# Performance work log

Hardware: AMD Instinct MI355X
Metric: run time of the kernel (lower is better)

## Reference

```python
import jax, jax.numpy as jnp
import numpy as np

H = 512      # hidden_size
L = 3        # num_layers
V = 4        # vocab / input_size
E = 64       # embedding_dim
B = 64       # batch
T = 512      # sequence length


def _rnn_layer(xs, h0, w_ih, w_hh, b_ih, b_hh):
    # xs: [T, B, D_in], h0: [B, H] -> (ys [T,B,H], hT [B,H])
    def step(h, x):
        h_new = jnp.tanh(x @ w_ih.T + b_ih + h @ w_hh.T + b_hh)
        return h_new, h_new
    hT, ys = jax.lax.scan(step, h0, xs)
    return ys, hT


def setup_inputs() -> dict:
    key = jax.random.key(0)
    ks = jax.random.split(key, 12)
    s = 1.0 / np.sqrt(H)  # torch RNN default init scale
    inp = {
        "x": jax.random.normal(ks[0], (B, T, V), dtype=jnp.float32),
        "emb": jax.random.normal(ks[1], (V, E), dtype=jnp.float32),
        # encoder RNN: layer 0 has input dim E, layers 1..2 have input dim H
        "enc_w_ih0": jax.random.uniform(ks[2], (H, E), jnp.float32, -s, s),
        "enc_w_ih_rest": jax.random.uniform(ks[3], (L - 1, H, H), jnp.float32, -s, s),
        "enc_w_hh": jax.random.uniform(ks[4], (L, H, H), jnp.float32, -s, s),
        "enc_b_ih": jax.random.uniform(ks[5], (L, H), jnp.float32, -s, s),
        "enc_b_hh": jax.random.uniform(ks[6], (L, H), jnp.float32, -s, s),
        # decoder RNN: all layers have input dim H
        "dec_w_ih": jax.random.uniform(ks[7], (L, H, H), jnp.float32, -s, s),
        "dec_w_hh": jax.random.uniform(ks[8], (L, H, H), jnp.float32, -s, s),
        "dec_b_ih": jax.random.uniform(ks[9], (L, H), jnp.float32, -s, s),
        "dec_b_hh": jax.random.uniform(ks[10], (L, H), jnp.float32, -s, s),
        "proj_w": jax.random.uniform(ks[11], (V, H), jnp.float32, -s, s),
    }
    return inp


def reference(x, emb, enc_w_ih0, enc_w_ih_rest, enc_w_hh, enc_b_ih, enc_b_hh,
              dec_w_ih, dec_w_hh, dec_b_ih, dec_b_hh, proj_w):
    # ---- Encoder ----
    # x_reduced_info slice is empty (FIRST_NONFUNCTIONAL_REDUCED_TOKEN_INDEX == len(VOCAB_REDUCED)),
    # so encoder RNN input is just the embedding of argmax(x).
    idx = jnp.argmax(x, axis=2)            # [B, T] int
    e = emb[idx]                           # [B, T, E]
    xs = jnp.transpose(e, (1, 0, 2))       # [T, B, E] (time-major for scan)

    h0 = jnp.zeros((B, H), dtype=x.dtype)
    enc_finals = []
    ys, hT = _rnn_layer(xs, h0, enc_w_ih0, enc_w_hh[0], enc_b_ih[0], enc_b_hh[0])
    enc_finals.append(hT)
    for l in range(1, L):
        ys, hT = _rnn_layer(ys, h0, enc_w_ih_rest[l - 1], enc_w_hh[l], enc_b_ih[l], enc_b_hh[l])
        enc_finals.append(hT)
    enc_h = jnp.stack(enc_finals, axis=0)  # [L, B, H]

    dec_h0 = jnp.flip(enc_h, axis=0)       # reverse_input_h=True
    x0 = jnp.zeros((B, H), dtype=x.dtype)

    def dec_step(carry, _):
        xin, hs = carry                    # xin [B,H], hs [L,B,H]
        new_hs = []
        cur = xin
        for l in range(L):
            h = jnp.tanh(cur @ dec_w_ih[l].T + dec_b_ih[l]
                         + hs[l] @ dec_w_hh[l].T + dec_b_hh[l])
            new_hs.append(h)
            cur = h
        out = jax.nn.log_softmax(cur @ proj_w.T, axis=-1)  # [B, V]
        return (cur, jnp.stack(new_hs, axis=0)), out

    _, outs = jax.lax.scan(dec_step, (x0, dec_h0), None, length=T)  # [T, B, V]
    return jnp.transpose(outs, (1, 0, 2))  # [B, T, V]
```

## Files before the change

kernel.cpp:

```cpp
#include <hip/hip_runtime.h>
#include <cmath>

#define HH 512
#define NV 4
#define ED 64
#define NB 64
#define NT 512

#define NWG  256
#define NTHR 512
#define WPG  32
#define RPG  8
#define CPW  16

#define HPAR (NB * HH)

#define IN0_OFF 0
#define IN1_OFF (8 * 1024)
#define LDS_FLOATS (IN1_OFF + 8 * 1024)
#define LDS_BYTES_ALLOC 98304

#define WS_INT_FLOATS 9216
#define FLAG(g, cb) (((g) * 32 + (cb)) * 32)

static __device__ __forceinline__ float gld(const float* p) {
  return __hip_atomic_load(p, __ATOMIC_RELAXED, __HIP_MEMORY_SCOPE_AGENT);
}
static __device__ __forceinline__ void gst(float* p, float v) {
  __hip_atomic_store(p, v, __ATOMIC_RELAXED, __HIP_MEMORY_SCOPE_AGENT);
}

static __device__ __forceinline__ void gbar(int* flags, int g, int cb, int ph) {
  asm volatile("s_waitcnt vmcnt(0)" ::: "memory");
  __syncthreads();
  if (threadIdx.x == 0)
    __hip_atomic_store(flags + FLAG(g, cb), ph, __ATOMIC_RELAXED,
                       __HIP_MEMORY_SCOPE_AGENT);
  if (threadIdx.x < 64) {
    const int* f = flags + FLAG(g, threadIdx.x & 31);
    while (__hip_atomic_load(f, __ATOMIC_RELAXED,
                             __HIP_MEMORY_SCOPE_AGENT) < ph)
      __builtin_amdgcn_s_sleep(1);
  }
  __syncthreads();
  asm volatile("" ::: "memory");
}

static __device__ __forceinline__ void gbar_all(int* ctr) {
  asm volatile("s_waitcnt vmcnt(0)" ::: "memory");
  __syncthreads();
  if (threadIdx.x == 0) {
    __hip_atomic_fetch_add(ctr, 1, __ATOMIC_RELAXED, __HIP_MEMORY_SCOPE_AGENT);
    while (__hip_atomic_load(ctr, __ATOMIC_RELAXED,
                             __HIP_MEMORY_SCOPE_AGENT) < NWG)
      __builtin_amdgcn_s_sleep(1);
  }
  __syncthreads();
  asm volatile("" ::: "memory");
}

template <bool COH>
static __device__ __forceinline__ void half_issue(const float* src, int row0,
                                                  float4 (&v)[2]) {
#pragma unroll
  for (int j = 0; j < 2; ++j) {
    const int qq = threadIdx.x + NTHR * j;
    const int row = qq >> 7, kq = qq & 127;
    const float* p = src + (size_t)(row0 + row) * HH + (kq << 2);
    if (COH) asm volatile("global_load_dwordx4 %0, %1, off sc0" : "=v"(v[j]) : "v"(p));
    else     asm volatile("global_load_dwordx4 %0, %1, off sc0 sc1" : "=v"(v[j]) : "v"(p));
  }
}
static __device__ __forceinline__ void half_commit(float* lds, int off,
                                                   int kofs, const float4 (&v)[2]) {
#pragma unroll
  for (int j = 0; j < 2; ++j) {
    const int qq = threadIdx.x + NTHR * j;
    const int row = qq >> 7, kq = qq & 127;
    *(float4*)(lds + off + row * 1024 + kofs + (kq << 2)) = v[j];
  }
}
static __device__ __forceinline__ void stage_half(float* lds, int off,
                                                  const float* src, int row0,
                                                  int kofs, int coh) {
  float4 v[2];
  if (coh) half_issue<true>(src, row0, v);
  else     half_issue<false>(src, row0, v);
  asm volatile("s_waitcnt vmcnt(0)" ::: "memory");
  __builtin_amdgcn_sched_barrier(0);
  half_commit(lds, off, kofs, v);
}

static __device__ __forceinline__ void unpk(float (&w)[16], int q, float4 v) {
  w[4*q+0] = v.x; w[4*q+1] = v.y; w[4*q+2] = v.z; w[4*q+3] = v.w;
}
static __device__ __forceinline__ void load_wq(float (&w)[16], const float* ih,
                                               const float* hh, int col, int ks) {
  unpk(w, 0, *(const float4*)(ih + (size_t)col * HH + ks * 4));
  unpk(w, 1, *(const float4*)(ih + (size_t)col * HH + 256 + ks * 4));
  unpk(w, 2, *(const float4*)(hh + (size_t)col * HH + ks * 4));
  unpk(w, 3, *(const float4*)(hh + (size_t)col * HH + 256 + ks * 4));
}
static __device__ __forceinline__ void load_wq0(float (&w)[16], const float* e,
                                                const float* hh, int col, int ks) {
  const float4 z = make_float4(0.f, 0.f, 0.f, 0.f);
  unpk(w, 0, (ks < 16) ? *(const float4*)(e + (size_t)col * ED + ks * 4)
                       : *(const float4*)(hh + (size_t)col * HH + (ks * 4 - 64)));
  unpk(w, 1, *(const float4*)(hh + (size_t)col * HH + 192 + ks * 4));
  unpk(w, 2, (ks < 16) ? *(const float4*)(hh + (size_t)col * HH + 448 + ks * 4) : z);
  unpk(w, 3, z);
}

static __device__ __forceinline__ void layer_tile(
    float* lds, int tile_off,
    const float (&wA)[16], const float (&wB)[16], float bA, float bB,
    float* dst, float* dst2, int row0, int colA, int coh) {
  const int lane = threadIdx.x & 63;
  const float* base = lds + tile_off + lane * 4;
  __syncthreads();
  float a[16];
#pragma unroll
  for (int v = 0; v < 16; ++v) a[v] = 0.f;
#pragma unroll
  for (int r = 0; r < 8; ++r) {
    const float* rb = base + r * 1024;
#pragma unroll
    for (int q = 0; q < 4; ++q) {
      const float4 iv = *(const float4*)(rb + q * 256);
      a[2*r+0] = fmaf(wA[4*q+0], iv.x, a[2*r+0]);
      a[2*r+0] = fmaf(wA[4*q+1], iv.y, a[2*r+0]);
      a[2*r+0] = fmaf(wA[4*q+2], iv.z, a[2*r+0]);
      a[2*r+0] = fmaf(wA[4*q+3], iv.w, a[2*r+0]);
      a[2*r+1] = fmaf(wB[4*q+0], iv.x, a[2*r+1]);
      a[2*r+1] = fmaf(wB[4*q+1], iv.y, a[2*r+1]);
      a[2*r+1] = fmaf(wB[4*q+2], iv.z, a[2*r+1]);
      a[2*r+1] = fmaf(wB[4*q+3], iv.w, a[2*r+1]);
    }
  }
  __syncthreads();
#pragma unroll
  for (int i = 0; i < 8; ++i) {
    const float send = (lane & 32) ? a[i] : a[i + 8];
    const float recv = __shfl_xor(send, 32);
    const float keep = (lane & 32) ? a[i + 8] : a[i];
    a[i] = keep + recv;
  }
#pragma unroll
  for (int i = 0; i < 4; ++i) {
    const float send = (lane & 16) ? a[i] : a[i + 4];
    const float recv = __shfl_xor(send, 16);
    const float keep = (lane & 16) ? a[i + 4] : a[i];
    a[i] = keep + recv;
  }
#pragma unroll
  for (int i = 0; i < 2; ++i) {
    const float send = (lane & 8) ? a[i] : a[i + 2];
    const float recv = __shfl_xor(send, 8);
    const float keep = (lane & 8) ? a[i + 2] : a[i];
    a[i] = keep + recv;
  }
  {
    const float send = (lane & 4) ? a[0] : a[1];
    const float recv = __shfl_xor(send, 4);
    const float keep = (lane & 4) ? a[1] : a[0];
    a[0] = keep + recv;
  }
  a[0] += __shfl_xor(a[0], 1);
  a[0] += __shfl_xor(a[0], 2);
  if ((lane & 3) == 0) {
    const int r  = ((lane >> 5) & 1) * 4 + ((lane >> 4) & 1) * 2 + ((lane >> 3) & 1);
    const int cc = (lane >> 2) & 1;
    const float h = tanhf(a[0] + (cc ? bB : bA));
    const size_t idx = (size_t)(row0 + r) * HH + colA + cc;
    if (coh) { dst[idx] = h; if (dst2) dst2[idx] = h; }
    else     { gst(dst + idx, h); if (dst2) gst(dst2 + idx, h); }
  }
}

static __device__ __forceinline__ void proj_row(const float* lds, int tile_off,
                                                int r_local, const float* projw,
                                                float* out, int row, int tt) {
  const int lane = threadIdx.x;
  const int v = lane & 3, kq = lane >> 2;
  float acc = 0.f;
#pragma unroll
  for (int i8 = 0; i8 < 8; ++i8) {
    const int k = (kq << 5) + (i8 << 2);
    const float4 iv = *(const float4*)(lds + tile_off + r_local * 1024 + k);
    const float4 wv = *(const float4*)(projw + (size_t)v * HH + k);
    acc = fmaf(iv.x, wv.x, acc);
    acc = fmaf(iv.y, wv.y, acc);
    acc = fmaf(iv.z, wv.z, acc);
    acc = fmaf(iv.w, wv.w, acc);
  }
  acc += __shfl_xor(acc, 4);
  acc += __shfl_xor(acc, 8);
  acc += __shfl_xor(acc, 16);
  acc += __shfl_xor(acc, 32);
  float m = fmaxf(acc, __shfl_xor(acc, 1));
  m = fmaxf(m, __shfl_xor(m, 2));
  const float e = expf(acc - m);
  float sum = e + __shfl_xor(e, 1);
  sum += __shfl_xor(sum, 2);
  const float res = acc - m - logf(sum);
  if (lane < 4) out[((size_t)row * NT + tt) * NV + lane] = res;
}

#define STG(off, src, kofs) stage_half(lds, off, src, row0, kofs, coh)
#define PF_ISSUE(src) \
  do { if (coh) half_issue<true>(src, row0, pf); \
       else     half_issue<false>(src, row0, pf); } while (0)

__global__ void __launch_bounds__(NTHR, 2) rnn_ae(
    const float* __restrict__ x, const float* __restrict__ emb,
    const float* __restrict__ ew_ih0, const float* __restrict__ ew_ihr,
    const float* __restrict__ ew_hh, const float* __restrict__ eb_ih,
    const float* __restrict__ eb_hh,
    const float* __restrict__ dw_ih, const float* __restrict__ dw_hh,
    const float* __restrict__ db_ih, const float* __restrict__ db_hh,
    const float* __restrict__ projw,
    float* __restrict__ out, float* __restrict__ ws) {
  extern __shared__ float lds[];

  const int tid = threadIdx.x;
  const int bid = blockIdx.x;
  const int g   = bid & 7;
  const int cb  = bid >> 3;
  const int row0 = g * RPG;
  const int col0 = cb * CPW;
  const int c   = tid >> 6;
  const int ks  = tid & 63;
  const int colA = col0 + 2 * c;
  const int colB = colA + 1;

  int* flags  = (int*)ws;
  int* gctr   = (int*)ws + 8192;
  int* xcdtab = (int*)ws + 8704;
  float* h0  = ws + WS_INT_FLOATS;
  float* h1  = h0 + 2 * HPAR;
  float* h2  = h1 + 2 * HPAR;
  float* e0  = h2 + 2 * HPAR;
  float* e1  = e0 + 2 * HPAR;
  float* e2  = e1 + 2 * HPAR;
  float* xfb = e2 + 2 * HPAR;
  int ph = 0;

  unsigned xcc;
  asm volatile("s_getreg_b32 %0, hwreg(HW_REG_XCC_ID)" : "=s"(xcc));
  if (tid == 0)
    __hip_atomic_store(xcdtab + bid, (int)xcc, __ATOMIC_RELAXED,
                       __HIP_MEMORY_SCOPE_AGENT);

  for (int i = tid; i < LDS_FLOATS; i += NTHR) lds[i] = 0.f;
  for (int i = cb * NTHR + tid; i < RPG * HH; i += WPG * NTHR) {
    const int r = i >> 9, cc = i & 511;
    const size_t o = HPAR + (size_t)(row0 + r) * HH + cc;
    gst(h0 + o, 0.f); gst(h1 + o, 0.f); gst(h2 + o, 0.f);
  }

  float wA0[16], wB0[16], wA1[16], wB1[16], wA2[16], wB2[16];
  float bA0, bB0, bA1, bB1, bA2, bB2;
  load_wq0(wA0, ew_ih0, ew_hh, colA, ks);
  load_wq0(wB0, ew_ih0, ew_hh, colB, ks);
  load_wq(wA1, ew_ihr,                ew_hh + (size_t)HH * HH,     colA, ks);
  load_wq(wB1, ew_ihr,                ew_hh + (size_t)HH * HH,     colB, ks);
  load_wq(wA2, ew_ihr + (size_t)HH * HH, ew_hh + (size_t)2 * HH * HH, colA, ks);
  load_wq(wB2, ew_ihr + (size_t)HH * HH, ew_hh + (size_t)2 * HH * HH, colB, ks);
  bA0 = eb_ih[0*HH + colA] + eb_hh[0*HH + colA];
  bB0 = eb_ih[0*HH + colB] + eb_hh[0*HH + colB];
  bA1 = eb_ih[1*HH + colA] + eb_hh[1*HH + colA];
  bB1 = eb_ih[1*HH + colB] + eb_hh[1*HH + colB];
  bA2 = eb_ih[2*HH + colA] + eb_hh[2*HH + colA];
  bB2 = eb_ih[2*HH + colB] + eb_hh[2*HH + colB];

  gbar_all(gctr);

  int coh = 1;
  {
    const int x0 = __hip_atomic_load(xcdtab + g, __ATOMIC_RELAXED,
                                     __HIP_MEMORY_SCOPE_AGENT);
    for (int j = 1; j < WPG; ++j)
      coh &= (__hip_atomic_load(xcdtab + g + 8 * j, __ATOMIC_RELAXED,
                                __HIP_MEMORY_SCOPE_AGENT) == x0);
  }

  for (int s = 0; s < NT + 2; ++s) {
    const int t = s, t1 = s - 1, t2 = s - 2;
    float4 v0[2], v1a[2], v1b[2], v2a[2], v2b[2];
    if (s < NT) {
      if (coh) half_issue<true>(h0 + ((t&1)^1) * HPAR, row0, v0);
      else     half_issue<false>(h0 + ((t&1)^1) * HPAR, row0, v0);
    }
    if (s >= 1 && s < NT + 1) {
      if (coh) { half_issue<true>(h0 + (t1&1) * HPAR, row0, v1a);
                 half_issue<true>(h1 + ((t1&1)^1) * HPAR, row0, v1b); }
      else     { half_issue<false>(h0 + (t1&1) * HPAR, row0, v1a);
                 half_issue<false>(h1 + ((t1&1)^1) * HPAR, row0, v1b); }
    }
    if (s >= 2) {
      if (coh) { half_issue<true>(h1 + (t2&1) * HPAR, row0, v2a);
                 half_issue<true>(h2 + ((t2&1)^1) * HPAR, row0, v2b); }
      else     { half_issue<false>(h1 + (t2&1) * HPAR, row0, v2a);
                 half_issue<false>(h2 + ((t2&1)^1) * HPAR, row0, v2b); }
    }
    asm volatile("s_waitcnt vmcnt(0)" ::: "memory");
    __builtin_amdgcn_sched_barrier(0);

    if (s < NT) {
      half_commit(lds, IN0_OFF, 64, v0);
      if (tid < 128) {
        const int r = tid >> 4, i8 = tid & 15;
        const float* xr = x + ((size_t)(row0 + r) * NT + t) * NV;
        const float a0 = xr[0], a1 = xr[1], a2 = xr[2], a3 = xr[3];
        int idx = 0; float m = a0;
        if (a1 > m) { m = a1; idx = 1; }
        if (a2 > m) { m = a2; idx = 2; }
        if (a3 > m) { m = a3; idx = 3; }
        const int k = i8 << 2;
        *(float4*)(lds + IN0_OFF + r * 1024 + k) =
            *(const float4*)(emb + idx * ED + k);
      }
    }
    if (s >= 1 && s < NT + 1) {
      half_commit(lds, IN1_OFF, 0,   v1a);
      half_commit(lds, IN1_OFF, 512, v1b);
    }
    if (s < NT)
      layer_tile(lds, IN0_OFF, wA0, wB0, bA0, bB0,
                 h0 + (t&1) * HPAR, nullptr, row0, colA, coh);
    if (s >= 1 && s < NT + 1)
      layer_tile(lds, IN1_OFF, wA1, wB1, bA1, bB1,
                 h1 + (t1&1) * HPAR, nullptr, row0, colA, coh);
    if (s >= 2) {
      half_commit(lds, IN1_OFF, 0,   v2a);
      half_commit(lds, IN1_OFF, 512, v2b);
      layer_tile(lds, IN1_OFF, wA2, wB2, bA2, bB2,
                 h2 + (t2&1) * HPAR, nullptr, row0, colA, coh);
    }
    gbar(flags, g, cb, ++ph);
  }

  for (int i = cb * NTHR + tid; i < RPG * HH; i += WPG * NTHR) {
    const int r = i >> 9, cc = i & 511;
    const size_t o = HPAR + (size_t)(row0 + r) * HH + cc;
    const float a = gld(h2 + o);
    const float b = gld(h1 + o);
    const float cv = gld(h0 + o);
    if (coh) { e0[o] = a; e1[o] = b; e2[o] = cv; xfb[o] = 0.f; }
    else     { gst(e0 + o, a); gst(e1 + o, b); gst(e2 + o, cv); gst(xfb + o, 0.f); }
  }
  load_wq(wA0, dw_ih,                     dw_hh,                     colA, ks);
  load_wq(wB0, dw_ih,                     dw_hh,                     colB, ks);
  load_wq(wA1, dw_ih + (size_t)HH * HH,   dw_hh + (size_t)HH * HH,   colA, ks);
  load_wq(wB1, dw_ih + (size_t)HH * HH,   dw_hh + (size_t)HH * HH,   colB, ks);
  load_wq(wA2, dw_ih + (size_t)2*HH*HH,   dw_hh + (size_t)2*HH*HH,   colA, ks);
  load_wq(wB2, dw_ih + (size_t)2*HH*HH,   dw_hh + (size_t)2*HH*HH,   colB, ks);
  bA0 = db_ih[0*HH + colA] + db_hh[0*HH + colA];
  bB0 = db_ih[0*HH + colB] + db_hh[0*HH + colB];
  bA1 = db_ih[1*HH + colA] + db_hh[1*HH + colA];
  bB1 = db_ih[1*HH + colB] + db_hh[1*HH + colB];
  bA2 = db_ih[2*HH + colA] + db_hh[2*HH + colA];
  bB2 = db_ih[2*HH + colB] + db_hh[2*HH + colB];
  gbar(flags, g, cb, ++ph);

  float4 pf[2];
  for (int t = 0; t < NT; ++t) {
    const int p = t & 1, q = p ^ 1;
    if (t == 0) STG(IN1_OFF, e0 + q * HPAR, 512);
    else        half_commit(lds, IN1_OFF, 512, pf);
    STG(IN1_OFF, xfb + q * HPAR, 0);
    __syncthreads();
    if (cb < 8 && tid < 64 && t >= 1)
      proj_row(lds, IN1_OFF, cb, projw, out, row0 + cb, t - 1);
    layer_tile(lds, IN1_OFF, wA0, wB0, bA0, bB0, e0 + p * HPAR, nullptr,
               row0, colA, coh);
    PF_ISSUE(e1 + q * HPAR);
    gbar(flags, g, cb, ++ph);

    half_commit(lds, IN1_OFF, 512, pf);
    STG(IN1_OFF, e0 + p * HPAR, 0);
    __syncthreads();
    layer_tile(lds, IN1_OFF, wA1, wB1, bA1, bB1, e1 + p * HPAR, nullptr,
               row0, colA, coh);
    PF_ISSUE(e2 + q * HPAR);
    gbar(flags, g, cb, ++ph);

    half_commit(lds, IN1_OFF, 512, pf);
    STG(IN1_OFF, e1 + p * HPAR, 0);
    __syncthreads();
    layer_tile(lds, IN1_OFF, wA2, wB2, bA2, bB2, e2 + p * HPAR,
               xfb + p * HPAR, row0, colA, coh);
    PF_ISSUE(e0 + p * HPAR);
    gbar(flags, g, cb, ++ph);
  }

  STG(IN1_OFF, xfb + ((NT - 1) & 1) * HPAR, 0);
  __syncthreads();
  if (cb < 8 && tid < 64)
    proj_row(lds, IN1_OFF, cb, projw, out, row0 + cb, NT - 1);
}

extern "C" void kernel_launch(void* const* d_in, const int* in_sizes, int n_in,
                              void* d_out, int out_size, void* d_ws, size_t ws_size,
                              hipStream_t stream) {
  const float* x      = (const float*)d_in[0];
  const float* emb    = (const float*)d_in[1];
  const float* ew_ih0 = (const float*)d_in[2];
  const float* ew_ihr = (const float*)d_in[3];
  const float* ew_hh  = (const float*)d_in[4];
  const float* eb_ih  = (const float*)d_in[5];
  const float* eb_hh  = (const float*)d_in[6];
  const float* dw_ih  = (const float*)d_in[7];
  const float* dw_hh  = (const float*)d_in[8];
  const float* db_ih  = (const float*)d_in[9];
  const float* db_hh  = (const float*)d_in[10];
  const float* projw  = (const float*)d_in[11];
  float* out = (float*)d_out;
  float* ws  = (float*)d_ws;

  (void)hipMemsetAsync(d_ws, 0, WS_INT_FLOATS * 4, stream);

  (void)hipFuncSetAttribute((const void*)rnn_ae,
                            hipFuncAttributeMaxDynamicSharedMemorySize,
                            LDS_BYTES_ALLOC);

  rnn_ae<<<dim3(NWG), dim3(NTHR), LDS_BYTES_ALLOC, stream>>>(
      x, emb, ew_ih0, ew_ihr, ew_hh, eb_ih, eb_hh,
      dw_ih, dw_hh, db_ih, db_hh, projw, out, ws);
}
```

Measured before the change: 7.873 ms.

## Split decoder barrier into arrive/wait and overlap recurrent half-dot with wait

```diff
diff --git a/kernel.cpp b/kernel.cpp
--- a/kernel.cpp
+++ b/kernel.cpp
@@ -30,12 +30,15 @@
   __hip_atomic_store(p, v, __ATOMIC_RELAXED, __HIP_MEMORY_SCOPE_AGENT);
 }
 
-static __device__ __forceinline__ void gbar(int* flags, int g, int cb, int ph) {
+static __device__ __forceinline__ void gbar_arrive(int* flags, int g, int cb,
+                                                   int ph) {
   asm volatile("s_waitcnt vmcnt(0)" ::: "memory");
   __syncthreads();
   if (threadIdx.x == 0)
     __hip_atomic_store(flags + FLAG(g, cb), ph, __ATOMIC_RELAXED,
                        __HIP_MEMORY_SCOPE_AGENT);
+}
+static __device__ __forceinline__ void gbar_wait(int* flags, int g, int ph) {
   if (threadIdx.x < 64) {
     const int* f = flags + FLAG(g, threadIdx.x & 31);
     while (__hip_atomic_load(f, __ATOMIC_RELAXED,
@@ -44,6 +47,10 @@
   }
   __syncthreads();
   asm volatile("" ::: "memory");
+}
+static __device__ __forceinline__ void gbar(int* flags, int g, int cb, int ph) {
+  gbar_arrive(flags, g, cb, ph);
+  gbar_wait(flags, g, ph);
 }
 
 static __device__ __forceinline__ void gbar_all(int* ctr) {
@@ -91,6 +98,10 @@
   half_commit(lds, off, kofs, v);
 }
 
+#define PF_DRAIN() \
+  do { asm volatile("s_waitcnt vmcnt(0)" ::: "memory"); \
+       __builtin_amdgcn_sched_barrier(0); } while (0)
+
 static __device__ __forceinline__ void unpk(float (&w)[16], int q, float4 v) {
   w[4*q+0] = v.x; w[4*q+1] = v.y; w[4*q+2] = v.z; w[4*q+3] = v.w;
 }
@@ -111,21 +122,17 @@
   unpk(w, 3, z);
 }
 
-static __device__ __forceinline__ void layer_tile(
-    float* lds, int tile_off,
-    const float (&wA)[16], const float (&wB)[16], float bA, float bB,
-    float* dst, float* dst2, int row0, int colA, int coh) {
+static __device__ __forceinline__ void tile_acc2(
+    float (&a)[16], const float* lds, int tile_off, int q0,
+    const float (&wA)[16], const float (&wB)[16]) {
   const int lane = threadIdx.x & 63;
   const float* base = lds + tile_off + lane * 4;
-  __syncthreads();
-  float a[16];
-#pragma unroll
-  for (int v = 0; v < 16; ++v) a[v] = 0.f;
 #pragma unroll
   for (int r = 0; r < 8; ++r) {
     const float* rb = base + r * 1024;
 #pragma unroll
-    for (int q = 0; q < 4; ++q) {
+    for (int qq = 0; qq < 2; ++qq) {
+      const int q = q0 + qq;
       const float4 iv = *(const float4*)(rb + q * 256);
       a[2*r+0] = fmaf(wA[4*q+0], iv.x, a[2*r+0]);
       a[2*r+0] = fmaf(wA[4*q+1], iv.y, a[2*r+0]);
@@ -137,7 +144,16 @@
       a[2*r+1] = fmaf(wB[4*q+3], iv.w, a[2*r+1]);
     }
   }
-  __syncthreads();
+}
+static __device__ __forceinline__ void zero16(float (&a)[16]) {
+#pragma unroll
+  for (int v = 0; v < 16; ++v) a[v] = 0.f;
+}
+
+static __device__ __forceinline__ void tile_finish(
+    float (&a)[16], float bA, float bB,
+    float* dst, float* dst2, int row0, int colA, int coh) {
+  const int lane = threadIdx.x & 63;
 #pragma unroll
   for (int i = 0; i < 8; ++i) {
     const float send = (lane & 32) ? a[i] : a[i + 8];
@@ -175,6 +191,19 @@
     if (coh) { dst[idx] = h; if (dst2) dst2[idx] = h; }
     else     { gst(dst + idx, h); if (dst2) gst(dst2 + idx, h); }
   }
+}
+
+static __device__ __forceinline__ void layer_tile(
+    float* lds, int tile_off,
+    const float (&wA)[16], const float (&wB)[16], float bA, float bB,
+    float* dst, float* dst2, int row0, int colA, int coh) {
+  __syncthreads();
+  float a[16];
+  zero16(a);
+  tile_acc2(a, lds, tile_off, 0, wA, wB);
+  tile_acc2(a, lds, tile_off, 2, wA, wB);
+  __syncthreads();
+  tile_finish(a, bA, bB, dst, dst2, row0, colA, coh);
 }
 
 static __device__ __forceinline__ void proj_row(const float* lds, int tile_off,
@@ -364,14 +393,11 @@
   gbar(flags, g, cb, ++ph);
 
   float4 pf[2];
-  for (int t = 0; t < NT; ++t) {
-    const int p = t & 1, q = p ^ 1;
-    if (t == 0) STG(IN1_OFF, e0 + q * HPAR, 512);
-    else        half_commit(lds, IN1_OFF, 512, pf);
+  {
+    const int p = 0, q = 1;
+    STG(IN1_OFF, e0 + q * HPAR, 512);
     STG(IN1_OFF, xfb + q * HPAR, 0);
     __syncthreads();
-    if (cb < 8 && tid < 64 && t >= 1)
-      proj_row(lds, IN1_OFF, cb, projw, out, row0 + cb, t - 1);
     layer_tile(lds, IN1_OFF, wA0, wB0, bA0, bB0, e0 + p * HPAR, nullptr,
                row0, colA, coh);
     PF_ISSUE(e1 + q * HPAR);
@@ -394,6 +420,52 @@
     gbar(flags, g, cb, ++ph);
   }
 
+  for (int t = 1; t < NT; ++t) {
+    const int p = t & 1, q = p ^ 1;
+
+    PF_DRAIN();
+    half_commit(lds, IN1_OFF, 512, pf);
+    __syncthreads();
+    float a0[16]; zero16(a0);
+    tile_acc2(a0, lds, IN1_OFF, 2, wA0, wB0);
+    gbar_wait(flags, g, ph);
+    STG(IN1_OFF, xfb + q * HPAR, 0);
+    __syncthreads();
+    if (cb < 8 && tid < 64)
+      proj_row(lds, IN1_OFF, cb, projw, out, row0 + cb, t - 1);
+    tile_acc2(a0, lds, IN1_OFF, 0, wA0, wB0);
+    tile_finish(a0, bA0, bB0, e0 + p * HPAR, nullptr, row0, colA, coh);
+    gbar_arrive(flags, g, cb, ++ph);
+    PF_ISSUE(e1 + q * HPAR);
+
+    PF_DRAIN();
+    half_commit(lds, IN1_OFF, 512, pf);
+    __syncthreads();
+    float a1[16]; zero16(a1);
+    tile_acc2(a1, lds, IN1_OFF, 2, wA1, wB1);
+    gbar_wait(flags, g, ph);
+    STG(IN1_OFF, e0 + p * HPAR, 0);
+    __syncthreads();
+    tile_acc2(a1, lds, IN1_OFF, 0, wA1, wB1);
+    tile_finish(a1, bA1, bB1, e1 + p * HPAR, nullptr, row0, colA, coh);
+    gbar_arrive(flags, g, cb, ++ph);
+    PF_ISSUE(e2 + q * HPAR);
+
+    PF_DRAIN();
+    half_commit(lds, IN1_OFF, 512, pf);
+    __syncthreads();
+    float a2[16]; zero16(a2);
+    tile_acc2(a2, lds, IN1_OFF, 2, wA2, wB2);
+    gbar_wait(flags, g, ph);
+    STG(IN1_OFF, e1 + p * HPAR, 0);
+    __syncthreads();
+    tile_acc2(a2, lds, IN1_OFF, 0, wA2, wB2);
+    tile_finish(a2, bA2, bB2, e2 + p * HPAR, xfb + p * HPAR, row0, colA, coh);
+    gbar_arrive(flags, g, cb, ++ph);
+    PF_ISSUE(e0 + p * HPAR);
+  }
+
+  gbar_wait(flags, g, ph);
   STG(IN1_OFF, xfb + ((NT - 1) & 1) * HPAR, 0);
   __syncthreads();
   if (cb < 8 && tid < 64)
```

Result: faster. 7.096 ms (-9.9%).
